# Kernel tuning notes

Measured on AMD Instinct MI355X. Metric: run time of the kernel, lower is better.

## Reference

```python
import math
import jax, jax.numpy as jnp
import numpy as np

B, H, N, D = 1, 16, 4096, 64
SINK_SIZE = 32
NUM_PROJS = 7
BLOCK_SIZE = 256
SAMPLE_SIZE = 256
MIN_SEQ_LEN = 1024
_SAMPLE_KEY = jax.random.key(1234)

def _hamming_perm(num_projs):
    a = np.array([0, 1])
    for _ in range(num_projs - 1):
        a = np.concatenate([a, a[::-1] + a.shape[0]])
    return jnp.asarray(a, dtype=jnp.int32)

_PERM = _hamming_perm(NUM_PROJS)
_MASK = jnp.asarray(2 ** np.arange(NUM_PROJS), dtype=jnp.int32)

def lsh_hash(x, proj_dir):
    # x: [b,h,n,d], proj_dir: [d,r] -> Gray-code-permuted bucket ids [b,h,n]
    rotated = jnp.einsum('bhnd,dr->bhnr', x, proj_dir)
    bin_ids = jnp.sum((rotated > 0).astype(jnp.int32) * _MASK, axis=-1)
    return _PERM[bin_ids]

def indexing(x, idx, chunk_size=-1):
    # gather rows along axis 2, optionally zero-pad to a multiple of chunk_size
    out = jnp.take_along_axis(x, idx[..., None], axis=2)
    if chunk_size > 0 and out.shape[2] % chunk_size != 0:
        pad = (-out.shape[2]) % chunk_size
        out = jnp.pad(out, ((0, 0), (0, 0), (0, pad), (0, 0)))
    return out

def exact_attention(q, k, v, scale, causal=False, bias=None):
    qk = jnp.einsum('bhqd,bhkd->bhqk', q, k) * scale
    if causal:
        nq, nk = q.shape[2], k.shape[2]
        cmask = jnp.triu(jnp.full((nq, nk), jnp.finfo(q.dtype).min, dtype=q.dtype), k=1)
        qk = qk + cmask
    if bias is not None:
        qk = qk + bias
    lse = jax.nn.logsumexp(qk, axis=-1, keepdims=True)
    attn = jnp.einsum('bhqk,bhkd->bhqd', jnp.exp(qk - lse), v)
    return attn, lse

def add_self_attentions(attn1, lse1, attn2, lse2):
    # attn = (attn1*e^lse1 + attn2*e^lse2)/(e^lse1+e^lse2); lse = log(e^lse1+e^lse2)
    c = jax.nn.sigmoid(lse1 - lse2)
    attn = c * attn1 + (1 - c) * attn2
    lse = jnp.logaddexp(lse1, lse2)
    return attn, lse

def forward_no_causal_mask(q, k, v, scale, proj_dir, ctr):
    b, h, nq, d = q.shape
    nk = k.shape[2]
    if MIN_SEQ_LEN > nq:
        return exact_attention(q, k, v, scale, causal=False)
    # 1) sortLSH block-diagonal attention
    q_sort_idx = jnp.argsort(lsh_hash(q, proj_dir), axis=2)  # stable
    k_sort_idx = jnp.argsort(lsh_hash(k, proj_dir), axis=2)
    q_sort_idx_inv = jnp.argsort(q_sort_idx, axis=2)
    q_sorted = indexing(q, q_sort_idx, BLOCK_SIZE)
    k_sorted = indexing(k, k_sort_idx, BLOCK_SIZE)
    v_sorted = indexing(v, k_sort_idx, BLOCK_SIZE)
    num_blocks = k_sorted.shape[2] // BLOCK_SIZE
    q_block = q_sorted.shape[2] // num_blocks
    qs = q_sorted.reshape(-1, 1, q_block, d)
    ks = k_sorted.reshape(-1, 1, BLOCK_SIZE, d)
    vs = v_sorted.reshape(-1, 1, BLOCK_SIZE, d)
    attn_block, lse_block = exact_attention(qs, ks, vs, scale, causal=False)
    attn_block = attn_block.reshape(b, h, q_sorted.shape[2], d)[:, :, :nq, :]
    lse_block = lse_block.reshape(b, h, q_sorted.shape[2], 1)[:, :, :nq, :]
    q_sorted = q_sorted[:, :, :nq, :]
    k_sorted = k_sorted[:, :, :nk, :]
    v_sorted = v_sorted[:, :, :nk, :]
    # 2) residual via uniform sampling (block-diag entries masked out)
    if SAMPLE_SIZE > 0 and nq > q_block and nk > BLOCK_SIZE:
        skey = jax.random.fold_in(_SAMPLE_KEY, ctr[0]); ctr[0] += 1
        sampled = jax.random.randint(skey, (b, h, SAMPLE_SIZE), 0, nk)
        v_sub = indexing(v_sorted, sampled)
        k_sub = indexing(k_sorted, sampled)
        q_blk_id = jnp.arange(nq) // q_block                 # [nq]
        k_blk_id = sampled // BLOCK_SIZE                     # [b,h,s]
        bias = (q_blk_id[None, None, :, None] == k_blk_id[:, :, None, :]).astype(q.dtype) * jnp.finfo(q.dtype).min
        attn_res, lse_res = exact_attention(q_sorted, k_sub, v_sub, scale, causal=False, bias=bias)
        lse_res = lse_res + math.log(nk / SAMPLE_SIZE)
        attn, lse = add_self_attentions(attn_block, lse_block, attn_res, lse_res)
    else:
        attn, lse = attn_block, lse_block
    # restore original row order
    attn = indexing(attn, q_sort_idx_inv)
    lse = indexing(lse, q_sort_idx_inv)
    return attn, lse

def hyper_causal(q, k, v, scale, proj_dir, ctr):
    b, h, n, d = q.shape
    if n <= MIN_SEQ_LEN:
        return exact_attention(q, k, v, scale, causal=True)
    n_orig = n
    if n % 2:
        q = jnp.pad(q, ((0, 0), (0, 0), (0, 1), (0, 0)))
        k = jnp.pad(k, ((0, 0), (0, 0), (0, 1), (0, 0)))
        v = jnp.pad(v, ((0, 0), (0, 0), (0, 1), (0, 0)))
    half = q.shape[2] // 2
    # recurse on the two diagonal halves (folded into head dim)
    attn_bd, lse_bd = hyper_causal(q.reshape(b, 2 * h, half, d), k.reshape(b, 2 * h, half, d), v.reshape(b, 2 * h, half, d), scale, proj_dir, ctr)
    attn_bd = attn_bd.reshape(b, h, -1, d)
    lse_bd = lse_bd.reshape(b, h, -1, 1)
    # off-diagonal lower-left block, unmasked
    attn_un, lse_un = forward_no_causal_mask(q[:, :, half:, :], k[:, :, :half, :], v[:, :, :half, :], scale, proj_dir, ctr)
    attn_up, lse_up = attn_bd[:, :, :half, :], lse_bd[:, :, :half, :]
    attn_dn, lse_dn = add_self_attentions(attn_bd[:, :, half:, :], lse_bd[:, :, half:, :], attn_un, lse_un)
    attn = jnp.concatenate([attn_up, attn_dn], axis=2)
    lse = jnp.concatenate([lse_up, lse_dn], axis=2)
    if n_orig % 2:
        attn = attn[:, :, :-1, :]
        lse = lse[:, :, :-1, :]
    return attn, lse

def _forward(query, key, value, proj_dir):
    b, h, n, d = query.shape
    scale = d ** (-0.5)
    sink = min(SINK_SIZE, n)
    prefix_attn, prefix_lse = exact_attention(query, key[:, :, :sink, :], value[:, :, :sink, :], scale, causal=True)
    if sink >= n:
        return prefix_attn
    ctr = [0]
    tail_attn, tail_lse = hyper_causal(query[:, :, sink:, :], key[:, :, sink:, :], value[:, :, sink:, :], scale, proj_dir, ctr)
    padded_tail_attn = jnp.zeros_like(prefix_attn).at[:, :, sink:, :].set(tail_attn)
    neg_inf = jnp.full_like(prefix_lse[:, :, :sink, :], jnp.finfo(prefix_lse.dtype).min)
    padded_tail_lse = jnp.concatenate([neg_inf, tail_lse], axis=2)
    attn, _ = add_self_attentions(prefix_attn, prefix_lse, padded_tail_attn, padded_tail_lse)
    return attn

def setup_inputs() -> dict:
    rng = jax.random.key(0)
    k1, k2, k3, k4 = jax.random.split(rng, 4)
    return {
        'query': jax.random.normal(k1, (B, H, N, D), jnp.float32),
        'key': jax.random.normal(k2, (B, H, N, D), jnp.float32),
        'value': jax.random.normal(k3, (B, H, N, D), jnp.float32),
        'proj_dir': jax.random.normal(k4, (D, NUM_PROJS), jnp.float32),
    }

def reference(query, key, value, proj_dir):
    return _forward(query, key, value, proj_dir)
```

## Files before the change

kernel.cpp:

```cpp
#include <hip/hip_runtime.h>
#include <hip/hip_bf16.h>
#include <math.h>
#include <stdint.h>

#define H_ 16
#define N_ 4096
#define NT_ 4064
#define NL_ 2032
#define SINK_ 32
#define SAMP_ 256
#define SCALE_ 0.125f
#define QSCALE_ 0.18033688f
#define M0L2_ 11.5415606f
#define M0_ 8.0f
#define NEGBIG_ -3.0e38f
#define LOGOFF_L2_ 2.9886841f

typedef unsigned int uint;
typedef unsigned short ushort;
typedef short bf16x8 __attribute__((ext_vector_type(8)));
typedef float f32x4 __attribute__((ext_vector_type(4)));

union B8 { uint4 u; bf16x8 b; };

// ... 22 lines not shown

__device__ __forceinline__ uint32_t rotl32_(uint32_t v, uint32_t d) {
  return (v << d) | (v >> (32u - d));
}

__device__ inline void tf2x32(uint32_t k0, uint32_t k1, uint32_t& x0, uint32_t& x1) {
  uint32_t ks2 = k0 ^ k1 ^ 0x1BD11BDAu;
  x0 += k0; x1 += k1;
#define TFR(r) { x0 += x1; x1 = rotl32_(x1, r); x1 ^= x0; }
  TFR(13u) TFR(15u) TFR(26u) TFR(6u)
  x0 += k1;  x1 += ks2 + 1u;
  TFR(17u) TFR(29u) TFR(16u) TFR(24u)
  x0 += ks2; x1 += k0 + 2u;
  TFR(13u) TFR(15u) TFR(26u) TFR(6u)
  x0 += k0;  x1 += k1 + 3u;
  TFR(17u) TFR(29u) TFR(16u) TFR(24u)
  x0 += k1;  x1 += ks2 + 4u;
  TFR(13u) TFR(15u) TFR(26u) TFR(6u)
  x0 += ks2; x1 += k0 + 5u;
#undef TFR
}

__device__ __forceinline__ void nomax_sm(f32x4 s[4], float& ssum) {
#pragma unroll
  for (int st = 0; st < 4; ++st)
#pragma unroll
    for (int r = 0; r < 4; ++r) {
      s[st][r] = __builtin_exp2f(s[st][r]);
      ssum += s[st][r];
    }
}

__device__ __forceinline__ void pv_go(const f32x4 s[4], f32x4 o[4],
                                      const char* vbase, char* pw, int g) {
#pragma unroll
  for (int hk2 = 0; hk2 < 2; ++hk2) {
    const f32x4 pa = s[2 * hk2], pc = s[2 * hk2 + 1];
    *(uint2*)(pw + 8 * g)      = make_uint2(cvtpk(pa[0], pa[1]), cvtpk(pa[2], pa[3]));
    *(uint2*)(pw + 32 + 8 * g) = make_uint2(cvtpk(pc[0], pc[1]), cvtpk(pc[2], pc[3]));
    B8 pf, vf;
    pf.u = *(const uint4*)(pw + g * 16);
    vf.u = *(const uint4*)(vbase + 0 * 2304 + hk2 * 64); o[0] = mfma16(vf, pf, o[0]);
    vf.u = *(const uint4*)(vbase + 1 * 2304 + hk2 * 64); o[1] = mfma16(vf, pf, o[1]);
    vf.u = *(const uint4*)(vbase + 2 * 2304 + hk2 * 64); o[2] = mfma16(vf, pf, o[2]);
    vf.u = *(const uint4*)(vbase + 3 * 2304 + hk2 * 64); o[3] = mfma16(vf, pf, o[3]);
  }
}

__global__ __launch_bounds__(256) void kern_packhash(
    const float* __restrict__ K, const float* __restrict__ V, const float* __restrict__ Q,
    const float* __restrict__ proj,
    ushort* __restrict__ Kb, ushort* __restrict__ Vb,
    int* __restrict__ hq, int* __restrict__ hk) {
  const int bb = blockIdx.x;
  if (bb < 4096) {
    const int which = bb >> 11;
    const size_t idx = ((size_t)(bb & 2047)) * 256 + threadIdx.x;
    const float4* s = (const float4*)((which == 0 ? K : V) + idx * 8);
    float4 f0 = s[0], f1 = s[1];
    uint4 p = make_uint4(bfpack(f0.x, f0.y), bfpack(f0.z, f0.w),
                         bfpack(f1.x, f1.y), bfpack(f1.z, f1.w));
    *(uint4*)((which == 0 ? Kb : Vb) + idx * 8) = p;
    return;
  }
  const int u = bb - 4096;
  const int h = u & 15, tile = (u >> 4) & 7, which = u >> 7;
  __shared__ float pr[448];
  for (int t = threadIdx.x; t < 448; t += 256) pr[t] = proj[t];
  __syncthreads();
  const int i = tile * 256 + (int)threadIdx.x;
  if (i >= NL_) return;
  const int orig = (which == 0) ? (SINK_ + NL_ + i) : (SINK_ + i);
  const float4* x = (const float4*)((which == 0 ? Q : K) + ((size_t)h * N_ + orig) * 64);
  float xr[64];
#pragma unroll
  for (int d = 0; d < 16; ++d) {
    float4 g = x[d];
    xr[4*d+0] = g.x; xr[4*d+1] = g.y; xr[4*d+2] = g.z; xr[4*d+3] = g.w;
// ... 60 lines not shown
  }

  int* dst = (which == 0 ? q_sort : k_sort) + h * NL_;
  if (tid < 64) {
    const int c = tid;
    for (int j = 0; j < 32; ++j) {
      const int u = c * 32 + j;
      if (u < NL_) {
        const int k = keys8[u];
        const int pos = (bscan[k] - btot[k]) + M[c * 130 + k];
        M[c * 130 + k] += 1;
        dst[pos] = u;
        srt[pos] = (ushort)u;
      }
    }
  }
  __syncthreads();

  if (which == 1) {
    const int s = tid;
    uint32_t a0 = 0u, a1 = 0u; tf2x32(0u, 1234u, a0, a1);
    uint32_t b0 = 0u, b1 = 0u; tf2x32(a0, a1, b0, b1);
    uint32_t c0 = 0u, c1 = 1u; tf2x32(a0, a1, c0, c1);
    const uint32_t j = (uint32_t)(h * SAMP_ + s);
    uint32_t h0 = 0u, h1 = j; tf2x32(b0, b1, h0, h1);
    uint32_t l0 = 0u, l1 = j; tf2x32(c0, c1, l0, l1);
    const uint32_t Hb = h0 ^ h1, Lb = l0 ^ l1;
    const uint32_t off = ((Hb % 2032u) * 16u + (Lb % 2032u)) % 2032u;
    samp_pos[h * SAMP_ + s] = (int)off;
    samp_orig[h * SAMP_ + s] = (int)srt[off];
  }
}

__global__ __launch_bounds__(256) void kern_attn_mfma(
    const float* __restrict__ Q, const ushort* __restrict__ Kb, const ushort* __restrict__ Vb,
    float* __restrict__ tail_attn, float* __restrict__ tail_lse,
    float* __restrict__ attn2, float* __restrict__ lse2) {
  __shared__ uint kk[4608];
  __shared__ uint vv[4608];
  __shared__ uint pbuf[1280];

  const int b = blockIdx.x;
  const int tid = threadIdx.x;
  const int lane = tid & 63, w = tid >> 6;
  const int g = lane >> 4, q = lane & 15;

  int h, q0, qbase, kbase, ntiles, p2vh = 0, chunkc = 0;
  bool causal;
  if (b < 256) {
    const int vh = b & 31; const int qt = b >> 5;
    h = vh >> 1; const int pp = vh & 1;
    q0 = qt * 128;
    qbase = SINK_ + pp * 2032 + 1016;
    kbase = SINK_ + pp * 2032;
    ntiles = 8; causal = false; p2vh = vh;
  } else {
    const int u = b - 256; const int vh = u & 63;
    const int qt = 7 - (u >> 6);
    h = vh >> 2; chunkc = vh & 3;
    q0 = qt * 128;
    qbase = SINK_ + chunkc * 1016;
    kbase = qbase;
    ntiles = qt + 1; causal = true;
  }
  const size_t hN = (size_t)h * N_;
  const int qrowA = q0 + w * 16 + q;
  const int qrowB = qrowA + 64;
  const int qcA = min(qrowA, 1015), qcB = min(qrowB, 1015);
  const int qwA_lo = q0 + w * 16, qwmaxA = qwA_lo + 15;
  const int qwB_lo = qwA_lo + 64;

  B8 qbA0, qbA1, qbB0, qbB1;
  {
    const float4* qp = (const float4*)(Q + (hN + qbase + qcA) * 64);
    float4 a = qp[2*g], c = qp[2*g+1], d = qp[8+2*g], e = qp[8+2*g+1];
    qbA0.u = make_uint4(bfpack(a.x*QSCALE_, a.y*QSCALE_), bfpack(a.z*QSCALE_, a.w*QSCALE_),
                        bfpack(c.x*QSCALE_, c.y*QSCALE_), bfpack(c.z*QSCALE_, c.w*QSCALE_));
    qbA1.u = make_uint4(bfpack(d.x*QSCALE_, d.y*QSCALE_), bfpack(d.z*QSCALE_, d.w*QSCALE_),
                        bfpack(e.x*QSCALE_, e.y*QSCALE_), bfpack(e.z*QSCALE_, e.w*QSCALE_));
    const float4* qp2 = (const float4*)(Q + (hN + qbase + qcB) * 64);
    a = qp2[2*g]; c = qp2[2*g+1]; d = qp2[8+2*g]; e = qp2[8+2*g+1];
    qbB0.u = make_uint4(bfpack(a.x*QSCALE_, a.y*QSCALE_), bfpack(a.z*QSCALE_, a.w*QSCALE_),
                        bfpack(c.x*QSCALE_, c.y*QSCALE_), bfpack(c.z*QSCALE_, c.w*QSCALE_));
    qbB1.u = make_uint4(bfpack(d.x*QSCALE_, d.y*QSCALE_), bfpack(d.z*QSCALE_, d.w*QSCALE_),
                        bfpack(e.x*QSCALE_, e.y*QSCALE_), bfpack(e.z*QSCALE_, e.w*QSCALE_));
  }
  f32x4 oA[4] = {{0,0,0,0},{0,0,0,0},{0,0,0,0},{0,0,0,0}};
  f32x4 oB[4] = {{0,0,0,0},{0,0,0,0},{0,0,0,0},{0,0,0,0}};
  float ssA = 0.f, ssB = 0.f;
  const f32x4 accb = {-M0L2_, -M0L2_, -M0L2_, -M0L2_};

  const int krow_l = tid >> 1, kpart = tid & 1;
  const int kpi = tid & 63;
  const int vdb = (tid >> 6) * 16;
  char* kdst = (char*)kk + krow_l * 144 + kpart * 64;
  char* vdst = (char*)vv + (kpi >> 5) * 9216 + vdb * 144 + (kpi & 31) * 4;
  const char* kq = (const char*)kk + q * 144 + g * 16;
  const char* vq = (const char*)vv + q * 144 + g * 16;
  char* pw = (char*)pbuf + w * 1280 + q * 80;

  const uint4 z4 = make_uint4(0, 0, 0, 0);
  uint4 kp0, kp1, kp2, kp3, va, va2, vb_, vb2;

#define LOADK(T) { const int kr = (T) * 128 + krow_l; \
    if (kr < 1016) { const uint4* s = (const uint4*)(Kb + (hN + kbase + kr) * 64 + kpart * 32); \
      kp0 = s[0]; kp1 = s[1]; kp2 = s[2]; kp3 = s[3]; } \
    else { kp0 = z4; kp1 = z4; kp2 = z4; kp3 = z4; } }
#define LOADV(T) { const int kr0 = (T) * 128 + 2 * kpi; \
    if (kr0 < 1016) { const uint4* s0 = (const uint4*)(Vb + (hN + kbase + kr0) * 64 + vdb); \
      const uint4* s1 = (const uint4*)(Vb + (hN + kbase + kr0 + 1) * 64 + vdb); \
      va = s0[0]; va2 = s0[1]; vb_ = s1[0]; vb2 = s1[1]; } \
    else { va = z4; va2 = z4; vb_ = z4; vb2 = z4; } }

  LOADK(0) LOADV(0)

  for (int t = 0; t < ntiles; ++t) {
    const int kt = t * 128;
    __syncthreads();
    *(uint4*)kdst = kp0; *(uint4*)(kdst + 16) = kp1;
    *(uint4*)(kdst + 32) = kp2; *(uint4*)(kdst + 48) = kp3;
#define VP(BASE, JW, AW, BW) { \
    *(uint*)(vdst + (BASE + 2*(JW)) * 144) = (AW & 0xffffu) | (BW << 16); \
    *(uint*)(vdst + (BASE + 2*(JW) + 1) * 144) = (AW >> 16) | (BW & 0xffff0000u); }
    VP(0, 0, va.x, vb_.x) VP(0, 1, va.y, vb_.y) VP(0, 2, va.z, vb_.z) VP(0, 3, va.w, vb_.w)
    VP(8, 0, va2.x, vb2.x) VP(8, 1, va2.y, vb2.y) VP(8, 2, va2.z, vb2.z) VP(8, 3, va2.w, vb2.w)
#undef VP
    __syncthreads();
    if (t + 1 < ntiles) { LOADK(t + 1) LOADV(t + 1) }

#pragma unroll
    for (int u2 = 0; u2 < 2; ++u2) {
      const int hb = kt + u2 * 64;
      const bool dA = !(causal && hb > qwmaxA);
      f32x4 sA[4], sB[4];
#pragma unroll
      for (int st = 0; st < 4; ++st) {
        B8 ka, kb2;
        ka.u  = *(const uint4*)(kq + (u2 * 64 + st * 16) * 144);
        kb2.u = *(const uint4*)(kq + (u2 * 64 + st * 16) * 144 + 64);
        if (dA) {
          f32x4 acc = accb;
          acc = mfma16(ka, qbA0, acc); acc = mfma16(kb2, qbA1, acc);
          sA[st] = acc;
        }
        f32x4 acc2 = accb;
        acc2 = mfma16(ka, qbB0, acc2); acc2 = mfma16(kb2, qbB1, acc2);
        sB[st] = acc2;
      }

      if (causal) {
        const int kb0 = hb + 4 * g;
        if (dA && hb + 63 > qwA_lo) {
#pragma unroll
          for (int st = 0; st < 4; ++st)
#pragma unroll
            for (int r = 0; r < 4; ++r)
              if (kb0 + st * 16 + r > qrowA) sA[st][r] = NEGBIG_;
        }
        if (hb + 63 > qwB_lo) {
#pragma unroll
          for (int st = 0; st < 4; ++st)
#pragma unroll
            for (int r = 0; r < 4; ++r)
              if (kb0 + st * 16 + r > qrowB) sB[st][r] = NEGBIG_;
        }
      } else if (hb + 63 >= 1016) {
        const int kb0 = hb + 4 * g;
#pragma unroll
        for (int st = 0; st < 4; ++st)
#pragma unroll
          for (int r = 0; r < 4; ++r)
            if (kb0 + st * 16 + r >= 1016) { sA[st][r] = NEGBIG_; sB[st][r] = NEGBIG_; }
      }

      if (dA) {
        nomax_sm(sA, ssA);
        pv_go(sA, oA, vq + u2 * 9216, pw, g);
      }
      nomax_sm(sB, ssB);
      pv_go(sB, oB, vq + u2 * 9216, pw, g);
    }
  }
#undef LOADK
#undef LOADV

  ssA += __shfl_xor(ssA, 16); ssA += __shfl_xor(ssA, 32);
  ssB += __shfl_xor(ssB, 16); ssB += __shfl_xor(ssB, 32);
#pragma unroll
  for (int fr = 0; fr < 2; ++fr) {
    const int qrow = fr == 0 ? qrowA : qrowB;
    if (qrow >= 1016) continue;
    f32x4* o = fr == 0 ? oA : oB;
    const float ss = fr == 0 ? ssA : ssB;
    const float lse = M0_ + __logf(ss);
    const float inv = 1.f / ss;
    if (causal) {
      const int trow = chunkc * 1016 + qrow;
      float* tp = tail_attn + ((size_t)h * NT_ + trow) * 64;
      *(f32x4*)(tp +  0 + 4*g) = o[0] * inv;
      *(f32x4*)(tp + 16 + 4*g) = o[1] * inv;
      *(f32x4*)(tp + 32 + 4*g) = o[2] * inv;
      *(f32x4*)(tp + 48 + 4*g) = o[3] * inv;
      if (lane < 16) tail_lse[h * NT_ + trow] = lse;
    } else {
      float* tp = attn2 + ((size_t)p2vh * 1016 + qrow) * 64;
      *(f32x4*)(tp +  0 + 4*g) = o[0] * inv;
      *(f32x4*)(tp + 16 + 4*g) = o[1] * inv;
      *(f32x4*)(tp + 32 + 4*g) = o[2] * inv;
      *(f32x4*)(tp + 48 + 4*g) = o[3] * inv;
      if (lane < 16) lse2[p2vh * 1016 + qrow] = lse;
    }
  }
}

__global__ __launch_bounds__(128) void kern_merge2(float* __restrict__ tail_attn, float* __restrict__ tail_lse,
                                                   const float* __restrict__ attn2, const float* __restrict__ lse2) {
  const int vh = blockIdx.x;
  const int i = blockIdx.y * 128 + (int)threadIdx.x;
  if (i >= 1016) return;
  const int h = vh >> 1, pp = vh & 1;
  const int t = pp * 2032 + 1016 + i;
  const float l2 = lse2[vh * 1016 + i];
  float* tlp = tail_lse + h * NT_ + t;
  const float bl = *tlp;
  const float c = 1.f / (1.f + __expf(l2 - bl));
  const float4* ap = (const float4*)(attn2 + ((size_t)vh * 1016 + i) * 64);
  float4* tp = (float4*)(tail_attn + ((size_t)h * NT_ + t) * 64);
#pragma unroll
  for (int d = 0; d < 16; ++d) {
    const float4 bd = tp[d], a2 = ap[d];
    tp[d] = make_float4(c * bd.x + (1.f - c) * a2.x,
                        c * bd.y + (1.f - c) * a2.y,
                        c * bd.z + (1.f - c) * a2.z,
                        c * bd.w + (1.f - c) * a2.w);
  }
  *tlp = logaddexpf_(bl, l2);
}

__global__ __launch_bounds__(256) void kern_lsh_mfma(
    const float* __restrict__ Q, const ushort* __restrict__ Kb, const ushort* __restrict__ Vb,
    const int* __restrict__ q_sort, const int* __restrict__ k_sort,
    const int* __restrict__ samp_pos, const int* __restrict__ samp_orig,
    float* __restrict__ tail_attn, float* __restrict__ tail_lse) {
  __shared__ uint kk[2304];
  __shared__ uint vv[2304];
  __shared__ uint pbuf[1280];
  __shared__ float bias_s[64];

  const int b = blockIdx.x;
  const int h = b >> 4, pt = b & 15;
  const int tid = threadIdx.x;
  const int lane = tid & 63, w = tid >> 6;
  const int g = lane >> 4, q = lane & 15;
  const int blkq = pt >> 1;
  const size_t hN = (size_t)h * N_;

  const int pA = pt * 128 + w * 16 + q;
  const int pB = pA + 64;
  const int qiA = q_sort[h * NL_ + min(pA, NL_ - 1)];
  const int qiB = q_sort[h * NL_ + min(pB, NL_ - 1)];

  const int skey = tid >> 2, kpart = tid & 3;
  const int kpi = tid & 31, vdb = (tid >> 5) * 8;
  int kidx[8], vi0[8], vi1[8];
#pragma unroll
  for (int t = 0; t < 8; ++t) {
    if (t < 4) {
      const int slot = blkq * 256 + t * 64 + skey;
      kidx[t] = (slot < NL_) ? k_sort[h * NL_ + slot] : -1;
      const int s0 = blkq * 256 + t * 64 + 2 * kpi;
      vi0[t] = (s0 < NL_) ? k_sort[h * NL_ + s0] : -1;
      vi1[t] = (s0 + 1 < NL_) ? k_sort[h * NL_ + s0 + 1] : -1;
    } else {
      kidx[t] = samp_orig[h * SAMP_ + (t - 4) * 64 + skey];
      const int si = (t - 4) * 64 + 2 * kpi;
      vi0[t] = samp_orig[h * SAMP_ + si];
      vi1[t] = samp_orig[h * SAMP_ + si + 1];
    }
  }
  float biasr[4];
  if (tid < 64) {
#pragma unroll
    for (int j = 0; j < 4; ++j)
      biasr[j] = ((samp_pos[h * SAMP_ + j * 64 + tid] >> 8) == blkq) ? NEGBIG_ : LOGOFF_L2_;
  }

  B8 qbA0, qbA1, qbB0, qbB1;
  {
    const float4* qp = (const float4*)(Q + (hN + SINK_ + NL_ + qiA) * 64);
    float4 a = qp[2*g], c = qp[2*g+1], d = qp[8+2*g], e = qp[8+2*g+1];
    qbA0.u = make_uint4(bfpack(a.x*QSCALE_, a.y*QSCALE_), bfpack(a.z*QSCALE_, a.w*QSCALE_),
                        bfpack(c.x*QSCALE_, c.y*QSCALE_), bfpack(c.z*QSCALE_, c.w*QSCALE_));
    qbA1.u = make_uint4(bfpack(d.x*QSCALE_, d.y*QSCALE_), bfpack(d.z*QSCALE_, d.w*QSCALE_),
                        bfpack(e.x*QSCALE_, e.y*QSCALE_), bfpack(e.z*QSCALE_, e.w*QSCALE_));
    const float4* qp2 = (const float4*)(Q + (hN + SINK_ + NL_ + qiB) * 64);
    a = qp2[2*g]; c = qp2[2*g+1]; d = qp2[8+2*g]; e = qp2[8+2*g+1];
    qbB0.u = make_uint4(bfpack(a.x*QSCALE_, a.y*QSCALE_), bfpack(a.z*QSCALE_, a.w*QSCALE_),
                        bfpack(c.x*QSCALE_, c.y*QSCALE_), bfpack(c.z*QSCALE_, c.w*QSCALE_));
    qbB1.u = make_uint4(bfpack(d.x*QSCALE_, d.y*QSCALE_), bfpack(d.z*QSCALE_, d.w*QSCALE_),
                        bfpack(e.x*QSCALE_, e.y*QSCALE_), bfpack(e.z*QSCALE_, e.w*QSCALE_));
  }
  f32x4 oA[4] = {{0,0,0,0},{0,0,0,0},{0,0,0,0},{0,0,0,0}};
  f32x4 oB[4] = {{0,0,0,0},{0,0,0,0},{0,0,0,0},{0,0,0,0}};
  float ssA = 0.f, ssB = 0.f;
  const f32x4 accb = {-M0L2_, -M0L2_, -M0L2_, -M0L2_};

  char* kdst = (char*)kk + skey * 144 + kpart * 32;
  char* vdst = (char*)vv + vdb * 144 + kpi * 4;
  const char* kq = (const char*)kk + q * 144 + g * 16;
  const char* vq = (const char*)vv + q * 144 + g * 16;
  char* pw = (char*)pbuf + w * 1280 + q * 80;

  const uint4 z4 = make_uint4(0, 0, 0, 0);
  uint4 kp0, kp1, va, vb_;

#define LLOADK(T) { const int kr = kidx[T]; \
    if (kr >= 0) { const uint4* s = (const uint4*)(Kb + (hN + SINK_ + kr) * 64 + kpart * 16); \
      kp0 = s[0]; kp1 = s[1]; } else { kp0 = z4; kp1 = z4; } }
#define LLOADV(T) { const int r0 = vi0[T], r1 = vi1[T]; \
    va  = (r0 >= 0) ? *(const uint4*)(Vb + (hN + SINK_ + r0) * 64 + vdb) : z4; \
    vb_ = (r1 >= 0) ? *(const uint4*)(Vb + (hN + SINK_ + r1) * 64 + vdb) : z4; }

  LLOADK(0) LLOADV(0)

  for (int t = 0; t < 8; ++t) {
    __syncthreads();
    *(uint4*)kdst = kp0; *(uint4*)(kdst + 16) = kp1;
#define VP(JW, AW, BW) { \
    *(uint*)(vdst + (2*(JW)) * 144) = (AW & 0xffffu) | (BW << 16); \
    *(uint*)(vdst + (2*(JW) + 1) * 144) = (AW >> 16) | (BW & 0xffff0000u); }
    VP(0, va.x, vb_.x) VP(1, va.y, vb_.y) VP(2, va.z, vb_.z) VP(3, va.w, vb_.w)
#undef VP
    if (t >= 4 && tid < 64) bias_s[tid] = biasr[t - 4];
    __syncthreads();
    if (t + 1 < 8) { LLOADK(t + 1) LLOADV(t + 1) }

    f32x4 sA[4], sB[4];
#pragma unroll
    for (int st = 0; st < 4; ++st) {
      B8 ka, kb2;
      ka.u  = *(const uint4*)(kq + (st * 16) * 144);
      kb2.u = *(const uint4*)(kq + (st * 16) * 144 + 64);
      f32x4 acc = accb;
      acc = mfma16(ka, qbA0, acc); acc = mfma16(kb2, qbA1, acc);
      sA[st] = acc;
      f32x4 acc2 = accb;
      acc2 = mfma16(ka, qbB0, acc2); acc2 = mfma16(kb2, qbB1, acc2);
      sB[st] = acc2;
    }
    if (t >= 4) {
      const f32x4* bp = (const f32x4*)bias_s;
#pragma unroll
      for (int st = 0; st < 4; ++st) {
        sA[st] = sA[st] + bp[st * 4 + g];
        sB[st] = sB[st] + bp[st * 4 + g];
      }
    }

    nomax_sm(sA, ssA);
    pv_go(sA, oA, vq, pw, g);
    nomax_sm(sB, ssB);
    pv_go(sB, oB, vq, pw, g);
  }
#undef LLOADK
#undef LLOADV

  ssA += __shfl_xor(ssA, 16); ssA += __shfl_xor(ssA, 32);
  ssB += __shfl_xor(ssB, 16); ssB += __shfl_xor(ssB, 32);
#pragma unroll
  for (int fr = 0; fr < 2; ++fr) {
    const int p = fr == 0 ? pA : pB;
    if (p >= NL_) continue;
    const int qi = fr == 0 ? qiA : qiB;
    f32x4* o = fr == 0 ? oA : oB;
    const float ss = fr == 0 ? ssA : ssB;
    const float un = M0_ + __logf(ss);
    const float inv = 1.f / ss;
    const int trow = NL_ + qi;
    float* tlp = tail_lse + h * NT_ + trow;
    const float bd = *tlp;
    const float c2 = 1.f / (1.f + __expf(un - bd));
    const float w2 = inv * (1.f - c2);
    float* tp = tail_attn + ((size_t)h * NT_ + trow) * 64;
    f32x4 t0 = *(f32x4*)(tp +  0 + 4*g);
    f32x4 t1 = *(f32x4*)(tp + 16 + 4*g);
    f32x4 t2 = *(f32x4*)(tp + 32 + 4*g);
    f32x4 t3 = *(f32x4*)(tp + 48 + 4*g);
    *(f32x4*)(tp +  0 + 4*g) = t0 * c2 + o[0] * w2;
    *(f32x4*)(tp + 16 + 4*g) = t1 * c2 + o[1] * w2;
    *(f32x4*)(tp + 32 + 4*g) = t2 * c2 + o[2] * w2;
    *(f32x4*)(tp + 48 + 4*g) = t3 * c2 + o[3] * w2;
    if (lane < 16) *tlp = logaddexpf_(bd, un);
  }
}

__global__ __launch_bounds__(256) void kern_final(const float* __restrict__ Q, const float* __restrict__ K,
                                                  const float* __restrict__ V,
                                                  const float* __restrict__ tail_attn, const float* __restrict__ tail_lse,
                                                  float* __restrict__ out) {
  const int h = blockIdx.x;
  const int r = blockIdx.y * 256 + (int)threadIdx.x;

  __shared__ float4 kk[SINK_ * 16];
  __shared__ float4 vv[SINK_ * 16];
  for (int u = threadIdx.x; u < SINK_ * 16; u += 256) {
    const int row = u >> 4, d4 = u & 15;
    kk[u] = ((const float4*)(K + ((size_t)h * N_ + row) * 64))[d4];
    vv[u] = ((const float4*)(V + ((size_t)h * N_ + row) * 64))[d4];
  }
  __syncthreads();

  float4 q4[16], acc[16];
  const float4* qp = (const float4*)(Q + ((size_t)h * N_ + r) * 64);
#pragma unroll
  for (int d = 0; d < 16; ++d) { q4[d] = qp[d]; acc[d] = make_float4(0.f, 0.f, 0.f, 0.f); }

  float m = -INFINITY, ssum = 0.f;
  const int nk = min(SINK_, r + 1);
  for (int j = 0; j < nk; ++j) {
    float s = 0.f;
#pragma unroll
    for (int d = 0; d < 16; ++d) {
      float4 x = q4[d], y = kk[j * 16 + d];
      s = fmaf(x.x, y.x, s); s = fmaf(x.y, y.y, s);
      s = fmaf(x.z, y.z, s); s = fmaf(x.w, y.w, s);
    }
    s *= SCALE_;
    const float nm = fmaxf(m, s);
    const float f = __expf(m - nm), wgt = __expf(s - nm);
    ssum = ssum * f + wgt;
    const float4* v4 = &vv[j * 16];
#pragma unroll
    for (int d = 0; d < 16; ++d) {
      acc[d].x = acc[d].x * f + wgt * v4[d].x;
      acc[d].y = acc[d].y * f + wgt * v4[d].y;
      acc[d].z = acc[d].z * f + wgt * v4[d].z;
      acc[d].w = acc[d].w * f + wgt * v4[d].w;
    }
    m = nm;
  }
  const float pl = m + __logf(ssum);
  const float inv = 1.f / ssum;
  float4* op = (float4*)(out + ((size_t)h * N_ + r) * 64);
  if (r < SINK_) {
#pragma unroll
    for (int d = 0; d < 16; ++d)
      op[d] = make_float4(acc[d].x * inv, acc[d].y * inv, acc[d].z * inv, acc[d].w * inv);
  } else {
    const int t = r - SINK_;
    const float tl = tail_lse[h * NT_ + t];
    const float cc = 1.f / (1.f + __expf(tl - pl));
    const float4* tp = (const float4*)(tail_attn + ((size_t)h * NT_ + t) * 64);
#pragma unroll
    for (int d = 0; d < 16; ++d) {
      const float4 tv = tp[d];
      op[d] = make_float4(cc * acc[d].x * inv + (1.f - cc) * tv.x,
                          cc * acc[d].y * inv + (1.f - cc) * tv.y,
                          cc * acc[d].z * inv + (1.f - cc) * tv.z,
                          cc * acc[d].w * inv + (1.f - cc) * tv.w);
    }
  }
}

extern "C" void kernel_launch(void* const* d_in, const int* in_sizes, int n_in,
                              void* d_out, int out_size, void* d_ws, size_t ws_size,
                              hipStream_t stream) {
  (void)in_sizes; (void)n_in; (void)out_size; (void)ws_size;
  const float* Q = (const float*)d_in[0];
  const float* K = (const float*)d_in[1];
  const float* V = (const float*)d_in[2];
  const float* proj = (const float*)d_in[3];
  float* out = (float*)d_out;

  char* w = (char*)d_ws;
  auto carve = [&](size_t bytes) { char* p = w; w += (bytes + 255) & ~(size_t)255; return p; };
  float* tail_attn = (float*)carve((size_t)H_ * NT_ * 64 * sizeof(float));
  float* tail_lse  = (float*)carve((size_t)H_ * NT_ * sizeof(float));
  float* attn2     = (float*)carve((size_t)32 * 1016 * 64 * sizeof(float));
  float* lse2      = (float*)carve((size_t)32 * 1016 * sizeof(float));
  ushort* Kb     = (ushort*)carve((size_t)H_ * N_ * 64 * sizeof(ushort));
  ushort* Vb     = (ushort*)carve((size_t)H_ * N_ * 64 * sizeof(ushort));
  int* hq        = (int*)carve((size_t)H_ * NL_ * sizeof(int));
  int* hk        = (int*)carve((size_t)H_ * NL_ * sizeof(int));
  int* q_sort    = (int*)carve((size_t)H_ * NL_ * sizeof(int));
  int* k_sort    = (int*)carve((size_t)H_ * NL_ * sizeof(int));
  int* samp_pos  = (int*)carve((size_t)H_ * SAMP_ * sizeof(int));
  int* samp_orig = (int*)carve((size_t)H_ * SAMP_ * sizeof(int));

  kern_packhash<<<dim3(4352), 256, 0, stream>>>(K, V, Q, proj, Kb, Vb, hq, hk);
  kern_sortsamp<<<dim3(H_, 2), 256, 0, stream>>>(hq, hk, q_sort, k_sort, samp_pos, samp_orig);
  kern_attn_mfma<<<dim3(768), 256, 0, stream>>>(Q, Kb, Vb, tail_attn, tail_lse, attn2, lse2);
  kern_merge2<<<dim3(32, 8), 128, 0, stream>>>(tail_attn, tail_lse, attn2, lse2);
  kern_lsh_mfma<<<dim3(256), 256, 0, stream>>>(Q, Kb, Vb, q_sort, k_sort, samp_pos, samp_orig,
                                               tail_attn, tail_lse);
  kern_final<<<dim3(H_, 16), 256, 0, stream>>>(Q, K, V, tail_attn, tail_lse, out);
}
```

Baseline: 159.0 us.

## Fuse LSH and causal attention kernels into one launch, defer merges to final

Merges the separate LSH block attention kernel into the main attention kernel as extra blocks, so both run in one launch. The LSH blocks now write their partial results to a new buffer instead of merging in place. The merge2 step and the LSH merge move into kern_final, which combines all partial results using their log-sum-exp values. This removes two launches and a serial dependency between them. The V and P shared-memory layouts are also changed: V rows now use a 272-byte stride, the P buffer is XOR-swizzled, and launch bounds are set to 4 blocks per CU. The cost is extra workspace memory and more global reads in the final kernel.

```diff
diff --git a/kernel.cpp b/kernel.cpp
--- a/kernel.cpp
+++ b/kernel.cpp
@@ -78,18 +78,21 @@
 }
 
 __device__ __forceinline__ void pv_go(const f32x4 s[4], f32x4 o[4],
-                                      const char* vbase, char* pw, int g) {
+                                      const char* vqb, char* pw, int g, int q, int keyoff) {
 #pragma unroll
   for (int hk2 = 0; hk2 < 2; ++hk2) {
     const f32x4 pa = s[2 * hk2], pc = s[2 * hk2 + 1];
-    *(uint2*)(pw + 8 * g)      = make_uint2(cvtpk(pa[0], pa[1]), cvtpk(pa[2], pa[3]));
-    *(uint2*)(pw + 32 + 8 * g) = make_uint2(cvtpk(pc[0], pc[1]), cvtpk(pc[2], pc[3]));
+    uint2 w0 = make_uint2(cvtpk(pa[0], pa[1]), cvtpk(pa[2], pa[3]));
+    uint2 w1 = make_uint2(cvtpk(pc[0], pc[1]), cvtpk(pc[2], pc[3]));
+    *(uint2*)(pw + ((((g >> 1)    ) ^ (q & 3)) * 16) + (g & 1) * 8) = w0;
+    *(uint2*)(pw + (((2 + (g >> 1)) ^ (q & 3)) * 16) + (g & 1) * 8) = w1;
     B8 pf, vf;
-    pf.u = *(const uint4*)(pw + g * 16);
-    vf.u = *(const uint4*)(vbase + 0 * 2304 + hk2 * 64); o[0] = mfma16(vf, pf, o[0]);
-    vf.u = *(const uint4*)(vbase + 1 * 2304 + hk2 * 64); o[1] = mfma16(vf, pf, o[1]);
-    vf.u = *(const uint4*)(vbase + 2 * 2304 + hk2 * 64); o[2] = mfma16(vf, pf, o[2]);
-    vf.u = *(const uint4*)(vbase + 3 * 2304 + hk2 * 64); o[3] = mfma16(vf, pf, o[3]);
+    pf.u = *(const uint4*)(pw + ((g ^ (q & 3)) * 16));
+    const int vo = keyoff + hk2 * 64;
+    vf.u = *(const uint4*)(vqb + 0 * 4352 + vo); o[0] = mfma16(vf, pf, o[0]);
+    vf.u = *(const uint4*)(vqb + 1 * 4352 + vo); o[1] = mfma16(vf, pf, o[1]);
+    vf.u = *(const uint4*)(vqb + 2 * 4352 + vo); o[2] = mfma16(vf, pf, o[2]);
+    vf.u = *(const uint4*)(vqb + 3 * 4352 + vo); o[3] = mfma16(vf, pf, o[3]);
   }
 }
 
@@ -216,30 +219,165 @@
   }
 }
 
-__global__ __launch_bounds__(256) void kern_attn_mfma(
+__global__ __launch_bounds__(256, 4) void kern_attn_fused(
     const float* __restrict__ Q, const ushort* __restrict__ Kb, const ushort* __restrict__ Vb,
+    const int* __restrict__ q_sort, const int* __restrict__ k_sort,
+    const int* __restrict__ samp_pos, const int* __restrict__ samp_orig,
     float* __restrict__ tail_attn, float* __restrict__ tail_lse,
-    float* __restrict__ attn2, float* __restrict__ lse2) {
+    float* __restrict__ attn2, float* __restrict__ lse2,
+    float* __restrict__ attn3, float* __restrict__ lse3) {
   __shared__ uint kk[4608];
-  __shared__ uint vv[4608];
-  __shared__ uint pbuf[1280];
+  __shared__ uint vv[4352];
+  __shared__ uint pbuf[1024];
+  __shared__ float bias_s[64];
 
   const int b = blockIdx.x;
   const int tid = threadIdx.x;
   const int lane = tid & 63, w = tid >> 6;
   const int g = lane >> 4, q = lane & 15;
+  const uint4 z4 = make_uint4(0, 0, 0, 0);
+  const f32x4 accb = {-M0L2_, -M0L2_, -M0L2_, -M0L2_};
+  char* pw = (char*)pbuf + w * 1024 + q * 64;
+  const char* kq = (const char*)kk + q * 144 + g * 16;
+  const char* vq = (const char*)vv + q * 272 + g * 16;
+
+  if (b < 256) {
+    const int h = b >> 4, pt = b & 15;
+    const int blkq = pt >> 1;
+    const size_t hN = (size_t)h * N_;
+
+    const int pA = pt * 128 + w * 16 + q;
+    const int pB = pA + 64;
+    const int qiA = q_sort[h * NL_ + min(pA, NL_ - 1)];
+    const int qiB = q_sort[h * NL_ + min(pB, NL_ - 1)];
+
+    const int skey = tid >> 2, kpart = tid & 3;
+    const int kpi = tid & 31, vdb = (tid >> 5) * 8;
+    char* kdst = (char*)kk + skey * 144 + kpart * 32;
+    char* vdst = (char*)vv + vdb * 272 + kpi * 4;
+
+    float biasr[4];
+    if (tid < 64) {
+#pragma unroll
+      for (int j = 0; j < 4; ++j)
+        biasr[j] = ((samp_pos[h * SAMP_ + j * 64 + tid] >> 8) == blkq) ? NEGBIG_ : LOGOFF_L2_;
+    }
+
+    B8 qbA0, qbA1, qbB0, qbB1;
+    {
+      const float4* qp = (const float4*)(Q + (hN + SINK_ + NL_ + qiA) * 64);
+      float4 a = qp[2*g], c = qp[2*g+1], d = qp[8+2*g], e = qp[8+2*g+1];
+      qbA0.u = make_uint4(bfpack(a.x*QSCALE_, a.y*QSCALE_), bfpack(a.z*QSCALE_, a.w*QSCALE_),
+                          bfpack(c.x*QSCALE_, c.y*QSCALE_), bfpack(c.z*QSCALE_, c.w*QSCALE_));
+      qbA1.u = make_uint4(bfpack(d.x*QSCALE_, d.y*QSCALE_), bfpack(d.z*QSCALE_, d.w*QSCALE_),
+                          bfpack(e.x*QSCALE_, e.y*QSCALE_), bfpack(e.z*QSCALE_, e.w*QSCALE_));
+      const float4* qp2 = (const float4*)(Q + (hN + SINK_ + NL_ + qiB) * 64);
+      a = qp2[2*g]; c = qp2[2*g+1]; d = qp2[8+2*g]; e = qp2[8+2*g+1];
+      qbB0.u = make_uint4(bfpack(a.x*QSCALE_, a.y*QSCALE_), bfpack(a.z*QSCALE_, a.w*QSCALE_),
+                          bfpack(c.x*QSCALE_, c.y*QSCALE_), bfpack(c.z*QSCALE_, c.w*QSCALE_));
+      qbB1.u = make_uint4(bfpack(d.x*QSCALE_, d.y*QSCALE_), bfpack(d.z*QSCALE_, d.w*QSCALE_),
+                          bfpack(e.x*QSCALE_, e.y*QSCALE_), bfpack(e.z*QSCALE_, e.w*QSCALE_));
+    }
+    f32x4 oA[4] = {{0,0,0,0},{0,0,0,0},{0,0,0,0},{0,0,0,0}};
+    f32x4 oB[4] = {{0,0,0,0},{0,0,0,0},{0,0,0,0},{0,0,0,0}};
+    float ssA = 0.f, ssB = 0.f;
+
+    int ck, cv0, cv1;
+    uint4 kp0, kp1, va, vb_;
+#define LIDX(T) { if ((T) < 4) { const int s0 = blkq * 256 + (T) * 64; \
+      const int sk = s0 + skey;   ck  = (sk < NL_) ? k_sort[h * NL_ + sk] : -1; \
+      const int sv = s0 + 2*kpi;  cv0 = (sv < NL_) ? k_sort[h * NL_ + sv] : -1; \
+                                  cv1 = (sv+1 < NL_) ? k_sort[h * NL_ + sv+1] : -1; \
+    } else { const int s0 = ((T) - 4) * 64; \
+      ck  = samp_orig[h * SAMP_ + s0 + skey]; \
+      cv0 = samp_orig[h * SAMP_ + s0 + 2*kpi]; \
+      cv1 = samp_orig[h * SAMP_ + s0 + 2*kpi + 1]; } }
+#define LKD() { if (ck >= 0) { const uint4* s = (const uint4*)(Kb + (hN + SINK_ + ck) * 64 + kpart * 16); \
+      kp0 = s[0]; kp1 = s[1]; } else { kp0 = z4; kp1 = z4; } }
+#define LVD() { va  = (cv0 >= 0) ? *(const uint4*)(Vb + (hN + SINK_ + cv0) * 64 + vdb) : z4; \
+                vb_ = (cv1 >= 0) ? *(const uint4*)(Vb + (hN + SINK_ + cv1) * 64 + vdb) : z4; }
+
+    LIDX(0) LKD() LVD()
+
+    for (int t = 0; t < 8; ++t) {
+      __syncthreads();
+      *(uint4*)kdst = kp0; *(uint4*)(kdst + 16) = kp1;
+#define VP(JW, AW, BW) { \
+      *(uint*)(vdst + (2*(JW)) * 272) = (AW & 0xffffu) | (BW << 16); \
+      *(uint*)(vdst + (2*(JW) + 1) * 272) = (AW >> 16) | (BW & 0xffff0000u); }
+      VP(0, va.x, vb_.x) VP(1, va.y, vb_.y) VP(2, va.z, vb_.z) VP(3, va.w, vb_.w)
+#undef VP
+      if (t >= 4 && tid < 64) bias_s[tid] = biasr[t - 4];
+      __syncthreads();
+      if (t + 1 < 8) {
+        const int tn = t + 1;
+        if (tn < 4) { LIDX(0 + tn) } else { LIDX(tn) }
+        LKD() LVD()
+      }
+
+      f32x4 sA[4], sB[4];
+#pragma unroll
+      for (int st = 0; st < 4; ++st) {
+        B8 ka, kb2;
+        ka.u  = *(const uint4*)(kq + (st * 16) * 144);
+        kb2.u = *(const uint4*)(kq + (st * 16) * 144 + 64);
+        f32x4 acc = accb;
+        acc = mfma16(ka, qbA0, acc); acc = mfma16(kb2, qbA1, acc);
+        sA[st] = acc;
+        f32x4 acc2 = accb;
+        acc2 = mfma16(ka, qbB0, acc2); acc2 = mfma16(kb2, qbB1, acc2);
+        sB[st] = acc2;
+      }
+      if (t >= 4) {
+        const f32x4* bp = (const f32x4*)bias_s;
+#pragma unroll
+        for (int st = 0; st < 4; ++st) {
+          sA[st] = sA[st] + bp[st * 4 + g];
+          sB[st] = sB[st] + bp[st * 4 + g];
+        }
+      }
+
+      nomax_sm(sA, ssA);
+      pv_go(sA, oA, vq, pw, g, q, 0);
+      nomax_sm(sB, ssB);
+      pv_go(sB, oB, vq, pw, g, q, 0);
+    }
+#undef LIDX
+#undef LKD
+#undef LVD
+
+    ssA += __shfl_xor(ssA, 16); ssA += __shfl_xor(ssA, 32);
+    ssB += __shfl_xor(ssB, 16); ssB += __shfl_xor(ssB, 32);
+#pragma unroll
+    for (int fr = 0; fr < 2; ++fr) {
+      const int p = fr == 0 ? pA : pB;
+      if (p >= NL_) continue;
+      const int qi = fr == 0 ? qiA : qiB;
+      f32x4* o = fr == 0 ? oA : oB;
+      const float ss = fr == 0 ? ssA : ssB;
+      const float un = M0_ + __logf(ss);
+      const float inv = 1.f / ss;
+      float* tp = attn3 + ((size_t)h * NL_ + qi) * 64;
+      *(f32x4*)(tp +  0 + 4*g) = o[0] * inv;
+      *(f32x4*)(tp + 16 + 4*g) = o[1] * inv;
+      *(f32x4*)(tp + 32 + 4*g) = o[2] * inv;
+      *(f32x4*)(tp + 48 + 4*g) = o[3] * inv;
+      if (lane < 16) lse3[h * NL_ + qi] = un;
+    }
+    return;
+  }
 
   int h, q0, qbase, kbase, ntiles, p2vh = 0, chunkc = 0;
   bool causal;
-  if (b < 256) {
-    const int vh = b & 31; const int qt = b >> 5;
+  if (b < 512) {
+    const int u = b - 256; const int vh = u & 31; const int qt = u >> 5;
     h = vh >> 1; const int pp = vh & 1;
     q0 = qt * 128;
     qbase = SINK_ + pp * 2032 + 1016;
     kbase = SINK_ + pp * 2032;
     ntiles = 8; causal = false; p2vh = vh;
   } else {
-    const int u = b - 256; const int vh = u & 63;
+    const int u = b - 512; const int vh = u & 63;
     const int qt = 7 - (u >> 6);
     h = vh >> 2; chunkc = vh & 3;
     q0 = qt * 128;
@@ -272,18 +410,13 @@
   f32x4 oA[4] = {{0,0,0,0},{0,0,0,0},{0,0,0,0},{0,0,0,0}};
   f32x4 oB[4] = {{0,0,0,0},{0,0,0,0},{0,0,0,0},{0,0,0,0}};
   float ssA = 0.f, ssB = 0.f;
-  const f32x4 accb = {-M0L2_, -M0L2_, -M0L2_, -M0L2_};
 
   const int krow_l = tid >> 1, kpart = tid & 1;
   const int kpi = tid & 63;
   const int vdb = (tid >> 6) * 16;
   char* kdst = (char*)kk + krow_l * 144 + kpart * 64;
-  char* vdst = (char*)vv + (kpi >> 5) * 9216 + vdb * 144 + (kpi & 31) * 4;
-  const char* kq = (const char*)kk + q * 144 + g * 16;
-  const char* vq = (const char*)vv + q * 144 + g * 16;
-  char* pw = (char*)pbuf + w * 1280 + q * 80;
-
-  const uint4 z4 = make_uint4(0, 0, 0, 0);
+  char* vdst = (char*)vv + vdb * 272 + kpi * 4;
+
   uint4 kp0, kp1, kp2, kp3, va, va2, vb_, vb2;
 
 #define LOADK(T) { const int kr = (T) * 128 + krow_l; \
@@ -304,8 +437,8 @@
     *(uint4*)kdst = kp0; *(uint4*)(kdst + 16) = kp1;
     *(uint4*)(kdst + 32) = kp2; *(uint4*)(kdst + 48) = kp3;
 #define VP(BASE, JW, AW, BW) { \
-    *(uint*)(vdst + (BASE + 2*(JW)) * 144) = (AW & 0xffffu) | (BW << 16); \
-    *(uint*)(vdst + (BASE + 2*(JW) + 1) * 144) = (AW >> 16) | (BW & 0xffff0000u); }
+    *(uint*)(vdst + (BASE + 2*(JW)) * 272) = (AW & 0xffffu) | (BW << 16); \
+    *(uint*)(vdst + (BASE + 2*(JW) + 1) * 272) = (AW >> 16) | (BW & 0xffff0000u); }
     VP(0, 0, va.x, vb_.x) VP(0, 1, va.y, vb_.y) VP(0, 2, va.z, vb_.z) VP(0, 3, va.w, vb_.w)
     VP(8, 0, va2.x, vb2.x) VP(8, 1, va2.y, vb2.y) VP(8, 2, va2.z, vb2.z) VP(8, 3, va2.w, vb2.w)
 #undef VP
@@ -359,10 +492,10 @@
 
       if (dA) {
         nomax_sm(sA, ssA);
-        pv_go(sA, oA, vq + u2 * 9216, pw, g);
+        pv_go(sA, oA, vq, pw, g, q, u2 * 128);
       }
       nomax_sm(sB, ssB);
-      pv_go(sB, oB, vq + u2 * 9216, pw, g);
+      pv_go(sB, oB, vq, pw, g, q, u2 * 128);
     }
   }
 #undef LOADK
@@ -397,191 +530,12 @@
   }
 }
 
-__global__ __launch_bounds__(128) void kern_merge2(float* __restrict__ tail_attn, float* __restrict__ tail_lse,
-                                                   const float* __restrict__ attn2, const float* __restrict__ lse2) {
-  const int vh = blockIdx.x;
-  const int i = blockIdx.y * 128 + (int)threadIdx.x;
-  if (i >= 1016) return;
-  const int h = vh >> 1, pp = vh & 1;
-  const int t = pp * 2032 + 1016 + i;
-  const float l2 = lse2[vh * 1016 + i];
-  float* tlp = tail_lse + h * NT_ + t;
-  const float bl = *tlp;
-  const float c = 1.f / (1.f + __expf(l2 - bl));
-  const float4* ap = (const float4*)(attn2 + ((size_t)vh * 1016 + i) * 64);
-  float4* tp = (float4*)(tail_attn + ((size_t)h * NT_ + t) * 64);
-#pragma unroll
-  for (int d = 0; d < 16; ++d) {
-    const float4 bd = tp[d], a2 = ap[d];
-    tp[d] = make_float4(c * bd.x + (1.f - c) * a2.x,
-                        c * bd.y + (1.f - c) * a2.y,
-                        c * bd.z + (1.f - c) * a2.z,
-                        c * bd.w + (1.f - c) * a2.w);
-  }
-  *tlp = logaddexpf_(bl, l2);
-}
-
-__global__ __launch_bounds__(256) void kern_lsh_mfma(
-    const float* __restrict__ Q, const ushort* __restrict__ Kb, const ushort* __restrict__ Vb,
-    const int* __restrict__ q_sort, const int* __restrict__ k_sort,
-    const int* __restrict__ samp_pos, const int* __restrict__ samp_orig,
-    float* __restrict__ tail_attn, float* __restrict__ tail_lse) {
-  __shared__ uint kk[2304];
-  __shared__ uint vv[2304];
-  __shared__ uint pbuf[1280];
-  __shared__ float bias_s[64];
-
-  const int b = blockIdx.x;
-  const int h = b >> 4, pt = b & 15;
-  const int tid = threadIdx.x;
-  const int lane = tid & 63, w = tid >> 6;
-  const int g = lane >> 4, q = lane & 15;
-  const int blkq = pt >> 1;
-  const size_t hN = (size_t)h * N_;
-
-  const int pA = pt * 128 + w * 16 + q;
-  const int pB = pA + 64;
-  const int qiA = q_sort[h * NL_ + min(pA, NL_ - 1)];
-  const int qiB = q_sort[h * NL_ + min(pB, NL_ - 1)];
-
-  const int skey = tid >> 2, kpart = tid & 3;
-  const int kpi = tid & 31, vdb = (tid >> 5) * 8;
-  int kidx[8], vi0[8], vi1[8];
-#pragma unroll
-  for (int t = 0; t < 8; ++t) {
-    if (t < 4) {
-      const int slot = blkq * 256 + t * 64 + skey;
-      kidx[t] = (slot < NL_) ? k_sort[h * NL_ + slot] : -1;
-      const int s0 = blkq * 256 + t * 64 + 2 * kpi;
-      vi0[t] = (s0 < NL_) ? k_sort[h * NL_ + s0] : -1;
-      vi1[t] = (s0 + 1 < NL_) ? k_sort[h * NL_ + s0 + 1] : -1;
-    } else {
-      kidx[t] = samp_orig[h * SAMP_ + (t - 4) * 64 + skey];
-      const int si = (t - 4) * 64 + 2 * kpi;
-      vi0[t] = samp_orig[h * SAMP_ + si];
-      vi1[t] = samp_orig[h * SAMP_ + si + 1];
-    }
-  }
-  float biasr[4];
-  if (tid < 64) {
-#pragma unroll
-    for (int j = 0; j < 4; ++j)
-      biasr[j] = ((samp_pos[h * SAMP_ + j * 64 + tid] >> 8) == blkq) ? NEGBIG_ : LOGOFF_L2_;
-  }
-
-  B8 qbA0, qbA1, qbB0, qbB1;
-  {
-    const float4* qp = (const float4*)(Q + (hN + SINK_ + NL_ + qiA) * 64);
-    float4 a = qp[2*g], c = qp[2*g+1], d = qp[8+2*g], e = qp[8+2*g+1];
-    qbA0.u = make_uint4(bfpack(a.x*QSCALE_, a.y*QSCALE_), bfpack(a.z*QSCALE_, a.w*QSCALE_),
-                        bfpack(c.x*QSCALE_, c.y*QSCALE_), bfpack(c.z*QSCALE_, c.w*QSCALE_));
-    qbA1.u = make_uint4(bfpack(d.x*QSCALE_, d.y*QSCALE_), bfpack(d.z*QSCALE_, d.w*QSCALE_),
-                        bfpack(e.x*QSCALE_, e.y*QSCALE_), bfpack(e.z*QSCALE_, e.w*QSCALE_));
-    const float4* qp2 = (const float4*)(Q + (hN + SINK_ + NL_ + qiB) * 64);
-    a = qp2[2*g]; c = qp2[2*g+1]; d = qp2[8+2*g]; e = qp2[8+2*g+1];
-    qbB0.u = make_uint4(bfpack(a.x*QSCALE_, a.y*QSCALE_), bfpack(a.z*QSCALE_, a.w*QSCALE_),
-                        bfpack(c.x*QSCALE_, c.y*QSCALE_), bfpack(c.z*QSCALE_, c.w*QSCALE_));
-    qbB1.u = make_uint4(bfpack(d.x*QSCALE_, d.y*QSCALE_), bfpack(d.z*QSCALE_, d.w*QSCALE_),
-                        bfpack(e.x*QSCALE_, e.y*QSCALE_), bfpack(e.z*QSCALE_, e.w*QSCALE_));
-  }
-  f32x4 oA[4] = {{0,0,0,0},{0,0,0,0},{0,0,0,0},{0,0,0,0}};
-  f32x4 oB[4] = {{0,0,0,0},{0,0,0,0},{0,0,0,0},{0,0,0,0}};
-  float ssA = 0.f, ssB = 0.f;
-  const f32x4 accb = {-M0L2_, -M0L2_, -M0L2_, -M0L2_};
-
-  char* kdst = (char*)kk + skey * 144 + kpart * 32;
-  char* vdst = (char*)vv + vdb * 144 + kpi * 4;
-  const char* kq = (const char*)kk + q * 144 + g * 16;
-  const char* vq = (const char*)vv + q * 144 + g * 16;
-  char* pw = (char*)pbuf + w * 1280 + q * 80;
-
-  const uint4 z4 = make_uint4(0, 0, 0, 0);
-  uint4 kp0, kp1, va, vb_;
-
-#define LLOADK(T) { const int kr = kidx[T]; \
-    if (kr >= 0) { const uint4* s = (const uint4*)(Kb + (hN + SINK_ + kr) * 64 + kpart * 16); \
-      kp0 = s[0]; kp1 = s[1]; } else { kp0 = z4; kp1 = z4; } }
-#define LLOADV(T) { const int r0 = vi0[T], r1 = vi1[T]; \
-    va  = (r0 >= 0) ? *(const uint4*)(Vb + (hN + SINK_ + r0) * 64 + vdb) : z4; \
-    vb_ = (r1 >= 0) ? *(const uint4*)(Vb + (hN + SINK_ + r1) * 64 + vdb) : z4; }
-
-  LLOADK(0) LLOADV(0)
-
-  for (int t = 0; t < 8; ++t) {
-    __syncthreads();
-    *(uint4*)kdst = kp0; *(uint4*)(kdst + 16) = kp1;
-#define VP(JW, AW, BW) { \
-    *(uint*)(vdst + (2*(JW)) * 144) = (AW & 0xffffu) | (BW << 16); \
-    *(uint*)(vdst + (2*(JW) + 1) * 144) = (AW >> 16) | (BW & 0xffff0000u); }
-    VP(0, va.x, vb_.x) VP(1, va.y, vb_.y) VP(2, va.z, vb_.z) VP(3, va.w, vb_.w)
-#undef VP
-    if (t >= 4 && tid < 64) bias_s[tid] = biasr[t - 4];
-    __syncthreads();
-    if (t + 1 < 8) { LLOADK(t + 1) LLOADV(t + 1) }
-
-    f32x4 sA[4], sB[4];
-#pragma unroll
-    for (int st = 0; st < 4; ++st) {
-      B8 ka, kb2;
-      ka.u  = *(const uint4*)(kq + (st * 16) * 144);
-      kb2.u = *(const uint4*)(kq + (st * 16) * 144 + 64);
-      f32x4 acc = accb;
-      acc = mfma16(ka, qbA0, acc); acc = mfma16(kb2, qbA1, acc);
-      sA[st] = acc;
-      f32x4 acc2 = accb;
-      acc2 = mfma16(ka, qbB0, acc2); acc2 = mfma16(kb2, qbB1, acc2);
-      sB[st] = acc2;
-    }
-    if (t >= 4) {
-      const f32x4* bp = (const f32x4*)bias_s;
-#pragma unroll
-      for (int st = 0; st < 4; ++st) {
-        sA[st] = sA[st] + bp[st * 4 + g];
-        sB[st] = sB[st] + bp[st * 4 + g];
-      }
-    }
-
-    nomax_sm(sA, ssA);
-    pv_go(sA, oA, vq, pw, g);
-    nomax_sm(sB, ssB);
-    pv_go(sB, oB, vq, pw, g);
-  }
-#undef LLOADK
-#undef LLOADV
-
-  ssA += __shfl_xor(ssA, 16); ssA += __shfl_xor(ssA, 32);
-  ssB += __shfl_xor(ssB, 16); ssB += __shfl_xor(ssB, 32);
-#pragma unroll
-  for (int fr = 0; fr < 2; ++fr) {
-    const int p = fr == 0 ? pA : pB;
-    if (p >= NL_) continue;
-    const int qi = fr == 0 ? qiA : qiB;
-    f32x4* o = fr == 0 ? oA : oB;
-    const float ss = fr == 0 ? ssA : ssB;
-    const float un = M0_ + __logf(ss);
-    const float inv = 1.f / ss;
-    const int trow = NL_ + qi;
-    float* tlp = tail_lse + h * NT_ + trow;
-    const float bd = *tlp;
-    const float c2 = 1.f / (1.f + __expf(un - bd));
-    const float w2 = inv * (1.f - c2);
-    float* tp = tail_attn + ((size_t)h * NT_ + trow) * 64;
-    f32x4 t0 = *(f32x4*)(tp +  0 + 4*g);
-    f32x4 t1 = *(f32x4*)(tp + 16 + 4*g);
-    f32x4 t2 = *(f32x4*)(tp + 32 + 4*g);
-    f32x4 t3 = *(f32x4*)(tp + 48 + 4*g);
-    *(f32x4*)(tp +  0 + 4*g) = t0 * c2 + o[0] * w2;
-    *(f32x4*)(tp + 16 + 4*g) = t1 * c2 + o[1] * w2;
-    *(f32x4*)(tp + 32 + 4*g) = t2 * c2 + o[2] * w2;
-    *(f32x4*)(tp + 48 + 4*g) = t3 * c2 + o[3] * w2;
-    if (lane < 16) *tlp = logaddexpf_(bd, un);
-  }
-}
-
-__global__ __launch_bounds__(256) void kern_final(const float* __restrict__ Q, const float* __restrict__ K,
-                                                  const float* __restrict__ V,
-                                                  const float* __restrict__ tail_attn, const float* __restrict__ tail_lse,
-                                                  float* __restrict__ out) {
+__global__ __launch_bounds__(256) void kern_final(
+    const float* __restrict__ Q, const float* __restrict__ K, const float* __restrict__ V,
+    const float* __restrict__ tail_attn, const float* __restrict__ tail_lse,
+    const float* __restrict__ attn2, const float* __restrict__ lse2,
+    const float* __restrict__ attn3, const float* __restrict__ lse3,
+    float* __restrict__ out) {
   const int h = blockIdx.x;
   const int r = blockIdx.y * 256 + (int)threadIdx.x;
 
@@ -630,20 +584,55 @@
 #pragma unroll
     for (int d = 0; d < 16; ++d)
       op[d] = make_float4(acc[d].x * inv, acc[d].y * inv, acc[d].z * inv, acc[d].w * inv);
-  } else {
-    const int t = r - SINK_;
-    const float tl = tail_lse[h * NT_ + t];
-    const float cc = 1.f / (1.f + __expf(tl - pl));
-    const float4* tp = (const float4*)(tail_attn + ((size_t)h * NT_ + t) * 64);
+    return;
+  }
+
+  const int t = r - SINK_;
+  float4 a[16];
+  const float4* tp = (const float4*)(tail_attn + ((size_t)h * NT_ + t) * 64);
+#pragma unroll
+  for (int d = 0; d < 16; ++d) a[d] = tp[d];
+  float al = tail_lse[h * NT_ + t];
+
+  const int pp = (t >= NL_) ? 1 : 0;
+  const int tloc = t - pp * NL_;
+  if (tloc >= 1016) {
+    const int vh = h * 2 + pp, i = tloc - 1016;
+    const float l2 = lse2[vh * 1016 + i];
+    const float c = 1.f / (1.f + __expf(l2 - al));
+    const float4* bp = (const float4*)(attn2 + ((size_t)vh * 1016 + i) * 64);
 #pragma unroll
     for (int d = 0; d < 16; ++d) {
-      const float4 tv = tp[d];
-      op[d] = make_float4(cc * acc[d].x * inv + (1.f - cc) * tv.x,
-                          cc * acc[d].y * inv + (1.f - cc) * tv.y,
-                          cc * acc[d].z * inv + (1.f - cc) * tv.z,
-                          cc * acc[d].w * inv + (1.f - cc) * tv.w);
-    }
-  }
+      const float4 bb = bp[d];
+      a[d] = make_float4(c * a[d].x + (1.f - c) * bb.x,
+                         c * a[d].y + (1.f - c) * bb.y,
+                         c * a[d].z + (1.f - c) * bb.z,
+                         c * a[d].w + (1.f - c) * bb.w);
+    }
+    al = logaddexpf_(al, l2);
+  }
+  if (t >= NL_) {
+    const int qi = t - NL_;
+    const float l3 = lse3[h * NL_ + qi];
+    const float c = 1.f / (1.f + __expf(l3 - al));
+    const float4* bp = (const float4*)(attn3 + ((size_t)h * NL_ + qi) * 64);
+#pragma unroll
+    for (int d = 0; d < 16; ++d) {
+      const float4 bb = bp[d];
+      a[d] = make_float4(c * a[d].x + (1.f - c) * bb.x,
+                         c * a[d].y + (1.f - c) * bb.y,
+                         c * a[d].z + (1.f - c) * bb.z,
+                         c * a[d].w + (1.f - c) * bb.w);
+    }
+    al = logaddexpf_(al, l3);
+  }
+  const float cc = 1.f / (1.f + __expf(al - pl));
+#pragma unroll
+  for (int d = 0; d < 16; ++d)
+    op[d] = make_float4(cc * acc[d].x * inv + (1.f - cc) * a[d].x,
+                        cc * acc[d].y * inv + (1.f - cc) * a[d].y,
+                        cc * acc[d].z * inv + (1.f - cc) * a[d].z,
+                        cc * acc[d].w * inv + (1.f - cc) * a[d].w);
 }
 
 extern "C" void kernel_launch(void* const* d_in, const int* in_sizes, int n_in,
@@ -662,6 +651,8 @@
   float* tail_lse  = (float*)carve((size_t)H_ * NT_ * sizeof(float));
   float* attn2     = (float*)carve((size_t)32 * 1016 * 64 * sizeof(float));
   float* lse2      = (float*)carve((size_t)32 * 1016 * sizeof(float));
+  float* attn3     = (float*)carve((size_t)H_ * NL_ * 64 * sizeof(float));
+  float* lse3      = (float*)carve((size_t)H_ * NL_ * sizeof(float));
   ushort* Kb     = (ushort*)carve((size_t)H_ * N_ * 64 * sizeof(ushort));
   ushort* Vb     = (ushort*)carve((size_t)H_ * N_ * 64 * sizeof(ushort));
   int* hq        = (int*)carve((size_t)H_ * NL_ * sizeof(int));
@@ -673,9 +664,8 @@
 
   kern_packhash<<<dim3(4352), 256, 0, stream>>>(K, V, Q, proj, Kb, Vb, hq, hk);
   kern_sortsamp<<<dim3(H_, 2), 256, 0, stream>>>(hq, hk, q_sort, k_sort, samp_pos, samp_orig);
-  kern_attn_mfma<<<dim3(768), 256, 0, stream>>>(Q, Kb, Vb, tail_attn, tail_lse, attn2, lse2);
-  kern_merge2<<<dim3(32, 8), 128, 0, stream>>>(tail_attn, tail_lse, attn2, lse2);
-  kern_lsh_mfma<<<dim3(256), 256, 0, stream>>>(Q, Kb, Vb, q_sort, k_sort, samp_pos, samp_orig,
-                                               tail_attn, tail_lse);
-  kern_final<<<dim3(H_, 16), 256, 0, stream>>>(Q, K, V, tail_attn, tail_lse, out);
-}
+  kern_attn_fused<<<dim3(1024), 256, 0, stream>>>(Q, Kb, Vb, q_sort, k_sort, samp_pos, samp_orig,
+                                                  tail_attn, tail_lse, attn2, lse2, attn3, lse3);
+  kern_final<<<dim3(H_, 16), 256, 0, stream>>>(Q, K, V, tail_attn, tail_lse,
+                                               attn2, lse2, attn3, lse3, out);
+}
```

Measured after the change: 310.4 us. 1.95x slower.
